# Kernel tuning notes

Hardware: AMD Instinct MI355X
Metric: run time of the kernel (lower is better)

The kernel has to match this reference:

```python
import jax, jax.numpy as jnp
import numpy as np

def setup_inputs() -> dict:
    key = jax.random.key(0)
    k1, k2, k3, k4 = jax.random.split(key, 4)
    B, T, D = 4, 4096, 256
    # xavier_normal_ with gain 0.002: std = 0.002 * sqrt(2/(D+D))
    std = 0.002 * np.sqrt(2.0 / (D + D))
    return {
        "x": jax.random.normal(k1, (B, T, D), dtype=jnp.float32),
        "W_k": jax.random.normal(k2, (D, D), dtype=jnp.float32) * std,
        "W_q": jax.random.normal(k3, (D, D), dtype=jnp.float32) * std,
        "W_v": jax.random.normal(k4, (D, D), dtype=jnp.float32) * std,
    }

def reference(x, W_k, W_q, W_v):
    # Projections: (B,T,D) @ (D,D) -> (B,T,D)
    K = jnp.einsum('btd,dk->btk', x, W_k)
    Q = jnp.einsum('btd,dq->btq', x, W_q)
    V = jnp.einsum('btd,dv->btv', x, W_v)
    # Note: original code has NO 1/sqrt(D) scaling.
    scores = jnp.einsum('bqd,bkd->bqk', Q, K)  # (B,T,T)
    attn = jax.nn.softmax(scores, axis=2)
    return jnp.einsum('bta,bav->btv', attn, V)
```

## Files before the change

### kernel.cpp

```cpp
#include <hip/hip_runtime.h>

typedef __attribute__((ext_vector_type(4))) float f32x4;
typedef __attribute__((ext_vector_type(8))) __bf16 bf16x8;
typedef __attribute__((ext_vector_type(4))) unsigned short u16x4;
typedef unsigned short u16;
typedef unsigned int u32;
typedef unsigned long long u64;

#define AS1 __attribute__((address_space(1)))
#define AS3 __attribute__((address_space(3)))

__device__ __forceinline__ void gload_lds16(const void* g, void* l) {
  __builtin_amdgcn_global_load_lds((const AS1 u32*)g, (AS3 u32*)l, 16, 0, 0);
}

__global__ __launch_bounds__(256) void k_flag(float* __restrict__ out, int n) {
  for (int i = blockIdx.x * 256 + threadIdx.x; i < n; i += gridDim.x * 256)
    out[i] = 1.0f;
}

__global__ __launch_bounds__(256) void k_cvt(const float* __restrict__ x,
                                             const float* __restrict__ Wk,
                                             const float* __restrict__ Wq,
                                             const float* __restrict__ Wv,
                                             __bf16* __restrict__ xb,
                                             __bf16* __restrict__ Wt) {
  int bx = blockIdx.x;
  if (bx < 2048) {
    int i = bx * 256 + threadIdx.x;
    const f32x4* p = (const f32x4*)x;
    f32x4 a = p[i * 2], b = p[i * 2 + 1];
    bf16x8 o;
    o[0] = (__bf16)a[0]; o[1] = (__bf16)a[1]; o[2] = (__bf16)a[2]; o[3] = (__bf16)a[3];
    o[4] = (__bf16)b[0]; o[5] = (__bf16)b[1]; o[6] = (__bf16)b[2]; o[7] = (__bf16)b[3];
    ((bf16x8*)xb)[i] = o;
  } else {
    int z = (bx - 2048) >> 8;
    const float* W = z == 0 ? Wk : (z == 1 ? Wq : Wv);
    int i = ((bx - 2048) & 255) * 256 + threadIdx.x;
    int n = i >> 8, k = i & 255;
    Wt[z * 65536 + i] = (__bf16)W[k * 256 + n];
  }
}

__global__ __launch_bounds__(256) void k_proj(const __bf16* __restrict__ xb,
                                              const __bf16* __restrict__ Wt,
                                              __bf16* __restrict__ Kb,
                                              __bf16* __restrict__ Qb,
                                              __bf16* __restrict__ Vt) {
  __shared__ __bf16 As[128 * 64];
  __shared__ __bf16 Bs[128 * 64];
  int tid = threadIdx.x;
  int lane = tid & 63, w = tid >> 6;
  int l15 = lane & 15, l4 = lane >> 4;
  int m0 = blockIdx.x * 128, n0 = blockIdx.y * 128;
  int z = blockIdx.z;
  const __bf16* Wz = Wt + z * 65536;
  int wm = (w & 1) * 64, wn = (w >> 1) * 64;
  f32x4 acc[4][4];
  for (int a = 0; a < 4; ++a)
    for (int b = 0; b < 4; ++b) acc[a][b] = (f32x4){0.f, 0.f, 0.f, 0.f};

  for (int k0 = 0; k0 < 256; k0 += 64) {
    __syncthreads();
    for (int it = 0; it < 4; ++it) {
      int id = it * 256 + tid;
      int r = id >> 3, c = id & 7, sc = c ^ (r & 7);
      gload_lds16(xb + (u64)(m0 + r) * 256 + k0 + sc * 8, (char*)As + id * 16);
    }
    for (int it = 0; it < 4; ++it) {
      int id = it * 256 + tid;
      int r = id >> 3, c = id & 7, sc = c ^ (r & 7);
      gload_lds16(Wz + (u64)(n0 + r) * 256 + k0 + sc * 8, (char*)Bs + id * 16);
    }
    asm volatile("s_waitcnt vmcnt(0)" ::: "memory");
    __syncthreads();
    for (int ks = 0; ks < 2; ++ks) {
      bf16x8 af[4], bg[4];
      for (int mf = 0; mf < 4; ++mf) {
        int m = wm + mf * 16 + l15;
        int ch = (ks * 4 + l4) ^ (m & 7);
        af[mf] = *(const bf16x8*)((const char*)As + m * 128 + ch * 16);
      }
      for (int nf = 0; nf < 4; ++nf) {
        int n = wn + nf * 16 + l15;
        int ch = (ks * 4 + l4) ^ (n & 7);
        bg[nf] = *(const bf16x8*)((const char*)Bs + n * 128 + ch * 16);
      }
      for (int mf = 0; mf < 4; ++mf)
        for (int nf = 0; nf < 4; ++nf)
          acc[mf][nf] = __builtin_amdgcn_mfma_f32_16x16x32_bf16(af[mf], bg[nf],
                                                                acc[mf][nf], 0, 0, 0);
    }
  }
  if (z != 2) {
    __bf16* C = z == 0 ? Kb : Qb;
    for (int mf = 0; mf < 4; ++mf)
      for (int nf = 0; nf < 4; ++nf)
        for (int r = 0; r < 4; ++r) {
          int m = m0 + wm + mf * 16 + l4 * 4 + r;
          int n = n0 + wn + nf * 16 + l15;
          C[(u64)m * 256 + n] = (__bf16)acc[mf][nf][r];
        }
  } else {
    int bb = m0 >> 12;
    for (int mf = 0; mf < 4; ++mf)
      for (int nf = 0; nf < 4; ++nf) {
        int n = n0 + wn + nf * 16 + l15;
        int tb = (m0 & 4095) + wm + mf * 16 + l4 * 4;
        u16x4 pk;
        for (int r = 0; r < 4; ++r) {
          __bf16 hh = (__bf16)acc[mf][nf][r];
          pk[r] = __builtin_bit_cast(u16, hh);
        }
        *(u16x4*)(Vt + (u64)bb * 1048576 + (u64)n * 4096 + tb) = pk;
      }
  }
}

#define KVB 32
__global__ __launch_bounds__(256) void k_attn(const __bf16* __restrict__ Qb,
                                              const __bf16* __restrict__ Kb,
                                              const __bf16* __restrict__ Vt,
                                              float* __restrict__ Out) {
  extern __shared__ char smem[];
  __bf16* Ks0 = (__bf16*)smem;
  __bf16* Ks1 = (__bf16*)(smem + 16384);
  __bf16* Vs0 = (__bf16*)(smem + 32768);
  __bf16* Vs1 = (__bf16*)(smem + 49152);
  __bf16* Ps  = (__bf16*)(smem + 65536);
  float*  Ls  = (float*)(smem + 69632);
  int tid = threadIdx.x, lane = tid & 63, w = tid >> 6;
  int l15 = lane & 15, l4 = lane >> 4;
  int s = w & 1, h = w >> 1;
  int id8 = blockIdx.x & 7, slot = blockIdx.x >> 3;
  int b = id8 >> 1;
  int q0 = (((id8 & 1) << 5) | slot) << 6;
  const __bf16* Kbb = Kb + (u64)b * 4096 * 256;
  const __bf16* Vtb = Vt + (u64)b * 1048576;

  bf16x8 qf[2][8];
  for (int mf = 0; mf < 2; ++mf) {
    const __bf16* Qrow = Qb + (u64)(b * 4096 + q0 + s * 32 + mf * 16 + l15) * 256;
    for (int ks = 0; ks < 8; ++ks) qf[mf][ks] = *(const bf16x8*)(Qrow + ks * 32 + l4 * 8);
  }

  f32x4 oacc[4][4];
  for (int a = 0; a < 4; ++a)
    for (int c = 0; c < 4; ++c) oacc[a][c] = (f32x4){0.f, 0.f, 0.f, 0.f};
  float lp[2][4] = {{0.f, 0.f, 0.f, 0.f}, {0.f, 0.f, 0.f, 0.f}};

  auto stageK = [&](int kv0, __bf16* dst) {
    for (int it = 0; it < 4; ++it) {
      int id = it * 256 + tid;
      int r = id >> 5, c = id & 31, sc = c ^ (r & 7);
      gload_lds16(Kbb + (u64)(kv0 + r) * 256 + sc * 8, (char*)dst + id * 16);
    }
  };
  auto stageV = [&](int kv0, __bf16* dst) {
    for (int it = 0; it < 4; ++it) {
      int id = it * 256 + tid;
      int d = id >> 2, c = id & 3, sc = c ^ (d & 3);
      gload_lds16(Vtb + (u64)d * 4096 + kv0 + sc * 8, (char*)dst + id * 16);
    }
  };

  stageK(0, Ks0);
  stageV(0, Vs0);
  asm volatile("s_waitcnt vmcnt(0)" ::: "memory");
  __syncthreads();

  for (int t = 0; t < 128; ++t) {
    __bf16* Kc = (t & 1) ? Ks1 : Ks0;
    __bf16* Vc = (t & 1) ? Vs1 : Vs0;
    __bf16* Kn = (t & 1) ? Ks0 : Ks1;
    __bf16* Vn = (t & 1) ? Vs0 : Vs1;
    if (t < 127) { stageK((t + 1) * KVB, Kn); stageV((t + 1) * KVB, Vn); }

    int kr = h * 16 + l15;
    f32x4 sa0 = (f32x4){0.f, 0.f, 0.f, 0.f}, sa1 = sa0, sb0 = sa0, sb1 = sa0;
    for (int ks = 0; ks < 8; ks += 2) {
      int ch0 = (ks * 4 + l4) ^ (kr & 7);
      int ch1 = ((ks + 1) * 4 + l4) ^ (kr & 7);
      bf16x8 kf0 = *(const bf16x8*)((const char*)Kc + kr * 512 + ch0 * 16);
      bf16x8 kf1 = *(const bf16x8*)((const char*)Kc + kr * 512 + ch1 * 16);
      sa0 = __builtin_amdgcn_mfma_f32_16x16x32_bf16(qf[0][ks], kf0, sa0, 0, 0, 0);
      sa1 = __builtin_amdgcn_mfma_f32_16x16x32_bf16(qf[1][ks], kf0, sa1, 0, 0, 0);
      sb0 = __builtin_amdgcn_mfma_f32_16x16x32_bf16(qf[0][ks + 1], kf1, sb0, 0, 0, 0);
      sb1 = __builtin_amdgcn_mfma_f32_16x16x32_bf16(qf[1][ks + 1], kf1, sb1, 0, 0, 0);
    }
    f32x4 sv[2] = {sa0 + sb0, sa1 + sb1};

    for (int mf = 0; mf < 2; ++mf)
      for (int r = 0; r < 4; ++r) {
        float p = __expf(sv[mf][r]);
        lp[mf][r] += p;
        int row = s * 32 + mf * 16 + l4 * 4 + r;
        int cs = (h * 2 + (l15 >> 3)) ^ l4;
        Ps[row * 32 + cs * 8 + (l15 & 7)] = (__bf16)p;
      }
    asm volatile("s_waitcnt lgkmcnt(0)\n\ts_barrier" ::: "memory");

    bf16x8 vf[4];
    for (int nf = 0; nf < 4; ++nf) {
      int d = w * 64 + nf * 16 + l15;
      int vc = l4 ^ (d & 3);
      vf[nf] = *(const bf16x8*)((const char*)Vc + d * 64 + vc * 16);
    }
    for (int mf = 0; mf < 4; ++mf) {
      int qr = mf * 16 + l15;
      int ch = l4 ^ ((l15 >> 2) & 3);
      bf16x8 pa = *(const bf16x8*)(Ps + qr * 32 + ch * 8);
      for (int nf = 0; nf < 4; ++nf)
        oacc[mf][nf] = __builtin_amdgcn_mfma_f32_16x16x32_bf16(pa, vf[nf], oacc[mf][nf], 0, 0, 0);
    }
    asm volatile("s_waitcnt vmcnt(0) lgkmcnt(0)\n\ts_barrier" ::: "memory");
  }

  for (int m = 1; m < 16; m <<= 1)
    for (int mf = 0; mf < 2; ++mf)
      for (int r = 0; r < 4; ++r) lp[mf][r] += __shfl_xor(lp[mf][r], m, 64);
  if (l15 == 0)
    for (int mf = 0; mf < 2; ++mf)
      for (int r = 0; r < 4; ++r)
        Ls[h * 64 + s * 32 + mf * 16 + l4 * 4 + r] = lp[mf][r];
  __syncthreads();

  float* Ob = Out + (u64)(b * 4096 + q0) * 256;
  for (int mf = 0; mf < 4; ++mf)
    for (int r = 0; r < 4; ++r) {
      int row = mf * 16 + l4 * 4 + r;
      float inv = 1.0f / (Ls[row] + Ls[64 + row]);
      for (int nf = 0; nf < 4; ++nf)
        Ob[(u64)row * 256 + w * 64 + nf * 16 + l15] = oacc[mf][nf][r] * inv;
    }
}

extern "C" void kernel_launch(void* const* d_in, const int* in_sizes, int n_in,
                              void* d_out, int out_size, void* d_ws, size_t ws_size,
                              hipStream_t stream) {
  const float* x  = (const float*)d_in[0];
  const float* Wk = (const float*)d_in[1];
  const float* Wq = (const float*)d_in[2];
  const float* Wv = (const float*)d_in[3];
  float* out = (float*)d_out;
  char* ws = (char*)d_ws;

  const size_t NEEDED = 25559040;
  if (ws_size < NEEDED) {
    k_flag<<<1024, 256, 0, stream>>>(out, out_size);
    return;
  }
  __bf16* Wt = (__bf16*)ws;
  __bf16* Kb = (__bf16*)(ws + 393216);
  __bf16* Qb = (__bf16*)(ws + 8781824);
  __bf16* Vt = (__bf16*)(ws + 17170432);
  __bf16* xb = (__bf16*)d_out;

  k_cvt<<<2816, 256, 0, stream>>>(x, Wk, Wq, Wv, xb, Wt);
  k_proj<<<dim3(128, 2, 3), 256, 0, stream>>>(xb, Wt, Kb, Qb, Vt);
  k_attn<<<256, 256, 70144, stream>>>(Qb, Kb, Vt, out);
}
```

Measured before the change: 214.4 us.

## Specialize attention warps into QK and PV groups, fuse x conversion into projection

The attention kernel now runs 8 waves: four compute QK^T and exp into a double-buffered P tile while the other four consume the previous step's P against V, so the two matmul phases overlap across waves with one barrier per step. The fp32-to-bf16 conversion of x moves into the projection GEMM's load path, removing a separate pass and the intermediate buffer. Projection tiles drop the XOR swizzle and async LDS loads in favour of padded shared memory and register-staged loads, and V is written transposed with swapped MFMA operands. The cost is more LDS, higher register pressure at 512 threads, and synchronous global loads in the projection.

```diff
diff --git a/kernel.cpp b/kernel.cpp
--- a/kernel.cpp
+++ b/kernel.cpp
@@ -2,7 +2,6 @@
 
 typedef __attribute__((ext_vector_type(4))) float f32x4;
 typedef __attribute__((ext_vector_type(8))) __bf16 bf16x8;
-typedef __attribute__((ext_vector_type(4))) unsigned short u16x4;
 typedef unsigned short u16;
 typedef unsigned int u32;
 typedef unsigned long long u64;
@@ -19,37 +18,23 @@
     out[i] = 1.0f;
 }
 
-__global__ __launch_bounds__(256) void k_cvt(const float* __restrict__ x,
-                                             const float* __restrict__ Wk,
-                                             const float* __restrict__ Wq,
-                                             const float* __restrict__ Wv,
-                                             __bf16* __restrict__ xb,
-                                             __bf16* __restrict__ Wt) {
-  int bx = blockIdx.x;
-  if (bx < 2048) {
-    int i = bx * 256 + threadIdx.x;
-    const f32x4* p = (const f32x4*)x;
-    f32x4 a = p[i * 2], b = p[i * 2 + 1];
-    bf16x8 o;
-    o[0] = (__bf16)a[0]; o[1] = (__bf16)a[1]; o[2] = (__bf16)a[2]; o[3] = (__bf16)a[3];
-    o[4] = (__bf16)b[0]; o[5] = (__bf16)b[1]; o[6] = (__bf16)b[2]; o[7] = (__bf16)b[3];
-    ((bf16x8*)xb)[i] = o;
-  } else {
-    int z = (bx - 2048) >> 8;
-    const float* W = z == 0 ? Wk : (z == 1 ? Wq : Wv);
-    int i = ((bx - 2048) & 255) * 256 + threadIdx.x;
-    int n = i >> 8, k = i & 255;
-    Wt[z * 65536 + i] = (__bf16)W[k * 256 + n];
-  }
-}
-
-__global__ __launch_bounds__(256) void k_proj(const __bf16* __restrict__ xb,
+__global__ __launch_bounds__(256) void k_cvt_w(const float* __restrict__ Wk,
+                                               const float* __restrict__ Wq,
+                                               const float* __restrict__ Wv,
+                                               __bf16* __restrict__ Wt) {
+  const float* W = blockIdx.y == 0 ? Wk : (blockIdx.y == 1 ? Wq : Wv);
+  int i = blockIdx.x * 256 + threadIdx.x;
+  int n = i >> 8, k = i & 255;
+  Wt[blockIdx.y * 65536 + i] = (__bf16)W[k * 256 + n];
+}
+
+__global__ __launch_bounds__(256) void k_proj(const float* __restrict__ x,
                                               const __bf16* __restrict__ Wt,
                                               __bf16* __restrict__ Kb,
                                               __bf16* __restrict__ Qb,
                                               __bf16* __restrict__ Vt) {
-  __shared__ __bf16 As[128 * 64];
-  __shared__ __bf16 Bs[128 * 64];
+  __shared__ __bf16 As[128][72];
+  __shared__ __bf16 Bs[128][72];
   int tid = threadIdx.x;
   int lane = tid & 63, w = tid >> 6;
   int l15 = lane & 15, l4 = lane >> 4;
@@ -64,33 +49,36 @@
   for (int k0 = 0; k0 < 256; k0 += 64) {
     __syncthreads();
     for (int it = 0; it < 4; ++it) {
-      int id = it * 256 + tid;
-      int r = id >> 3, c = id & 7, sc = c ^ (r & 7);
-      gload_lds16(xb + (u64)(m0 + r) * 256 + k0 + sc * 8, (char*)As + id * 16);
+      int id = it * 256 + tid, r = id >> 3, c = id & 7;
+      const float* src = x + (u64)(m0 + r) * 256 + k0 + c * 8;
+      f32x4 a = *(const f32x4*)src, b2 = *(const f32x4*)(src + 4);
+      bf16x8 o;
+      o[0] = (__bf16)a[0];  o[1] = (__bf16)a[1];  o[2] = (__bf16)a[2];  o[3] = (__bf16)a[3];
+      o[4] = (__bf16)b2[0]; o[5] = (__bf16)b2[1]; o[6] = (__bf16)b2[2]; o[7] = (__bf16)b2[3];
+      *(bf16x8*)&As[r][c * 8] = o;
     }
     for (int it = 0; it < 4; ++it) {
-      int id = it * 256 + tid;
-      int r = id >> 3, c = id & 7, sc = c ^ (r & 7);
-      gload_lds16(Wz + (u64)(n0 + r) * 256 + k0 + sc * 8, (char*)Bs + id * 16);
-    }
-    asm volatile("s_waitcnt vmcnt(0)" ::: "memory");
+      int id = it * 256 + tid, r = id >> 3, c = id & 7;
+      *(bf16x8*)&Bs[r][c * 8] = *(const bf16x8*)(Wz + (u64)(n0 + r) * 256 + k0 + c * 8);
+    }
     __syncthreads();
     for (int ks = 0; ks < 2; ++ks) {
       bf16x8 af[4], bg[4];
-      for (int mf = 0; mf < 4; ++mf) {
-        int m = wm + mf * 16 + l15;
-        int ch = (ks * 4 + l4) ^ (m & 7);
-        af[mf] = *(const bf16x8*)((const char*)As + m * 128 + ch * 16);
-      }
-      for (int nf = 0; nf < 4; ++nf) {
-        int n = wn + nf * 16 + l15;
-        int ch = (ks * 4 + l4) ^ (n & 7);
-        bg[nf] = *(const bf16x8*)((const char*)Bs + n * 128 + ch * 16);
-      }
       for (int mf = 0; mf < 4; ++mf)
-        for (int nf = 0; nf < 4; ++nf)
-          acc[mf][nf] = __builtin_amdgcn_mfma_f32_16x16x32_bf16(af[mf], bg[nf],
-                                                                acc[mf][nf], 0, 0, 0);
+        af[mf] = *(const bf16x8*)&As[wm + mf * 16 + l15][(ks * 4 + l4) * 8];
+      for (int nf = 0; nf < 4; ++nf)
+        bg[nf] = *(const bf16x8*)&Bs[wn + nf * 16 + l15][(ks * 4 + l4) * 8];
+      if (z != 2) {
+        for (int mf = 0; mf < 4; ++mf)
+          for (int nf = 0; nf < 4; ++nf)
+            acc[mf][nf] = __builtin_amdgcn_mfma_f32_16x16x32_bf16(af[mf], bg[nf],
+                                                                  acc[mf][nf], 0, 0, 0);
+      } else {
+        for (int mf = 0; mf < 4; ++mf)
+          for (int nf = 0; nf < 4; ++nf)
+            acc[mf][nf] = __builtin_amdgcn_mfma_f32_16x16x32_bf16(bg[nf], af[mf],
+                                                                  acc[mf][nf], 0, 0, 0);
+      }
     }
   }
   if (z != 2) {
@@ -105,34 +93,26 @@
   } else {
     int bb = m0 >> 12;
     for (int mf = 0; mf < 4; ++mf)
-      for (int nf = 0; nf < 4; ++nf) {
-        int n = n0 + wn + nf * 16 + l15;
-        int tb = (m0 & 4095) + wm + mf * 16 + l4 * 4;
-        u16x4 pk;
+      for (int nf = 0; nf < 4; ++nf)
         for (int r = 0; r < 4; ++r) {
-          __bf16 hh = (__bf16)acc[mf][nf][r];
-          pk[r] = __builtin_bit_cast(u16, hh);
-        }
-        *(u16x4*)(Vt + (u64)bb * 1048576 + (u64)n * 4096 + tb) = pk;
-      }
+          int n = n0 + wn + nf * 16 + l4 * 4 + r;
+          int t = (m0 & 4095) + wm + mf * 16 + l15;
+          Vt[(u64)bb * 1048576 + (u64)n * 4096 + t] = (__bf16)acc[mf][nf][r];
+        }
   }
 }
 
 #define KVB 32
-__global__ __launch_bounds__(256) void k_attn(const __bf16* __restrict__ Qb,
-                                              const __bf16* __restrict__ Kb,
-                                              const __bf16* __restrict__ Vt,
-                                              float* __restrict__ Out) {
+__global__ __launch_bounds__(512, 2) void k_attn(const __bf16* __restrict__ Qb,
+                                                 const __bf16* __restrict__ Kb,
+                                                 const __bf16* __restrict__ Vt,
+                                                 float* __restrict__ Out) {
   extern __shared__ char smem[];
-  __bf16* Ks0 = (__bf16*)smem;
-  __bf16* Ks1 = (__bf16*)(smem + 16384);
-  __bf16* Vs0 = (__bf16*)(smem + 32768);
-  __bf16* Vs1 = (__bf16*)(smem + 49152);
-  __bf16* Ps  = (__bf16*)(smem + 65536);
-  float*  Ls  = (float*)(smem + 69632);
+  float* Ls = (float*)(smem + 73728);
   int tid = threadIdx.x, lane = tid & 63, w = tid >> 6;
   int l15 = lane & 15, l4 = lane >> 4;
-  int s = w & 1, h = w >> 1;
+  bool isQK = (w < 4);
+  int s = w & 1, h = (w >> 1) & 1, w4 = w - 4;
   int id8 = blockIdx.x & 7, slot = blockIdx.x >> 3;
   int b = id8 >> 1;
   int q0 = (((id8 & 1) << 5) | slot) << 6;
@@ -140,100 +120,110 @@
   const __bf16* Vtb = Vt + (u64)b * 1048576;
 
   bf16x8 qf[2][8];
-  for (int mf = 0; mf < 2; ++mf) {
-    const __bf16* Qrow = Qb + (u64)(b * 4096 + q0 + s * 32 + mf * 16 + l15) * 256;
-    for (int ks = 0; ks < 8; ++ks) qf[mf][ks] = *(const bf16x8*)(Qrow + ks * 32 + l4 * 8);
-  }
+  if (isQK)
+    for (int mf = 0; mf < 2; ++mf) {
+      const __bf16* Qrow = Qb + (u64)(b * 4096 + q0 + s * 32 + mf * 16 + l15) * 256;
+      for (int ks = 0; ks < 8; ++ks) qf[mf][ks] = *(const bf16x8*)(Qrow + ks * 32 + l4 * 8);
+    }
 
   f32x4 oacc[4][4];
   for (int a = 0; a < 4; ++a)
     for (int c = 0; c < 4; ++c) oacc[a][c] = (f32x4){0.f, 0.f, 0.f, 0.f};
   float lp[2][4] = {{0.f, 0.f, 0.f, 0.f}, {0.f, 0.f, 0.f, 0.f}};
 
-  auto stageK = [&](int kv0, __bf16* dst) {
-    for (int it = 0; it < 4; ++it) {
-      int id = it * 256 + tid;
+  auto stageK = [&](int kv0, char* dst) {
+    for (int it = 0; it < 2; ++it) {
+      int id = it * 512 + tid;
       int r = id >> 5, c = id & 31, sc = c ^ (r & 7);
-      gload_lds16(Kbb + (u64)(kv0 + r) * 256 + sc * 8, (char*)dst + id * 16);
+      gload_lds16(Kbb + (u64)(kv0 + r) * 256 + sc * 8, dst + id * 16);
     }
   };
-  auto stageV = [&](int kv0, __bf16* dst) {
-    for (int it = 0; it < 4; ++it) {
-      int id = it * 256 + tid;
+  auto stageV = [&](int kv0, char* dst) {
+    for (int it = 0; it < 2; ++it) {
+      int id = it * 512 + tid;
       int d = id >> 2, c = id & 3, sc = c ^ (d & 3);
-      gload_lds16(Vtb + (u64)d * 4096 + kv0 + sc * 8, (char*)dst + id * 16);
+      gload_lds16(Vtb + (u64)d * 4096 + kv0 + sc * 8, dst + id * 16);
     }
   };
 
-  stageK(0, Ks0);
-  stageV(0, Vs0);
+  stageK(0, smem);
   asm volatile("s_waitcnt vmcnt(0)" ::: "memory");
   __syncthreads();
 
-  for (int t = 0; t < 128; ++t) {
-    __bf16* Kc = (t & 1) ? Ks1 : Ks0;
-    __bf16* Vc = (t & 1) ? Vs1 : Vs0;
-    __bf16* Kn = (t & 1) ? Ks0 : Ks1;
-    __bf16* Vn = (t & 1) ? Vs0 : Vs1;
-    if (t < 127) { stageK((t + 1) * KVB, Kn); stageV((t + 1) * KVB, Vn); }
-
-    int kr = h * 16 + l15;
-    f32x4 sa0 = (f32x4){0.f, 0.f, 0.f, 0.f}, sa1 = sa0, sb0 = sa0, sb1 = sa0;
-    for (int ks = 0; ks < 8; ks += 2) {
-      int ch0 = (ks * 4 + l4) ^ (kr & 7);
-      int ch1 = ((ks + 1) * 4 + l4) ^ (kr & 7);
-      bf16x8 kf0 = *(const bf16x8*)((const char*)Kc + kr * 512 + ch0 * 16);
-      bf16x8 kf1 = *(const bf16x8*)((const char*)Kc + kr * 512 + ch1 * 16);
-      sa0 = __builtin_amdgcn_mfma_f32_16x16x32_bf16(qf[0][ks], kf0, sa0, 0, 0, 0);
-      sa1 = __builtin_amdgcn_mfma_f32_16x16x32_bf16(qf[1][ks], kf0, sa1, 0, 0, 0);
-      sb0 = __builtin_amdgcn_mfma_f32_16x16x32_bf16(qf[0][ks + 1], kf1, sb0, 0, 0, 0);
-      sb1 = __builtin_amdgcn_mfma_f32_16x16x32_bf16(qf[1][ks + 1], kf1, sb1, 0, 0, 0);
-    }
-    f32x4 sv[2] = {sa0 + sb0, sa1 + sb1};
-
-    for (int mf = 0; mf < 2; ++mf)
+  for (int t = 0; t <= 128; ++t) {
+    char* KsC = smem + (t & 1) * 16384;
+    char* VsP = smem + 32768 + ((t + 1) & 1) * 16384;
+    char* PsC = smem + 65536 + (t & 1) * 4096;
+    char* PsP = smem + 65536 + ((t + 1) & 1) * 4096;
+    if (t < 127) stageK((t + 1) * KVB, smem + ((t + 1) & 1) * 16384);
+    if (t < 128) stageV(t * KVB, smem + 32768 + (t & 1) * 16384);
+
+    if (isQK) {
+      if (t < 128) {
+        int kr = h * 16 + l15;
+        f32x4 sa0 = (f32x4){0.f, 0.f, 0.f, 0.f}, sa1 = sa0, sb0 = sa0, sb1 = sa0;
+        for (int ks = 0; ks < 8; ks += 2) {
+          int ch0 = (ks * 4 + l4) ^ (kr & 7);
+          int ch1 = ((ks + 1) * 4 + l4) ^ (kr & 7);
+          bf16x8 kf0 = *(const bf16x8*)(KsC + kr * 512 + ch0 * 16);
+          bf16x8 kf1 = *(const bf16x8*)(KsC + kr * 512 + ch1 * 16);
+          sa0 = __builtin_amdgcn_mfma_f32_16x16x32_bf16(qf[0][ks], kf0, sa0, 0, 0, 0);
+          sa1 = __builtin_amdgcn_mfma_f32_16x16x32_bf16(qf[1][ks], kf0, sa1, 0, 0, 0);
+          sb0 = __builtin_amdgcn_mfma_f32_16x16x32_bf16(qf[0][ks + 1], kf1, sb0, 0, 0, 0);
+          sb1 = __builtin_amdgcn_mfma_f32_16x16x32_bf16(qf[1][ks + 1], kf1, sb1, 0, 0, 0);
+        }
+        f32x4 sv[2] = {sa0 + sb0, sa1 + sb1};
+        for (int mf = 0; mf < 2; ++mf)
+          for (int r = 0; r < 4; ++r) {
+            float p = __expf(sv[mf][r]);
+            lp[mf][r] += p;
+            int row = s * 32 + mf * 16 + l4 * 4 + r;
+            int cs = (h * 2 + (l15 >> 3)) ^ l4;
+            *(__bf16*)(PsC + row * 64 + cs * 16 + (l15 & 7) * 2) = (__bf16)p;
+          }
+      }
+    } else {
+      if (t >= 1) {
+        bf16x8 vf[4];
+        for (int nf = 0; nf < 4; ++nf) {
+          int d = w4 * 64 + nf * 16 + l15;
+          int vc = l4 ^ (d & 3);
+          vf[nf] = *(const bf16x8*)(VsP + d * 64 + vc * 16);
+        }
+        for (int mf = 0; mf < 4; ++mf) {
+          int qr = mf * 16 + l15;
+          int ch = l4 ^ ((l15 >> 2) & 3);
+          bf16x8 pa = *(const bf16x8*)(PsP + qr * 64 + ch * 16);
+          for (int nf = 0; nf < 4; ++nf)
+            oacc[mf][nf] = __builtin_amdgcn_mfma_f32_16x16x32_bf16(pa, vf[nf],
+                                                                   oacc[mf][nf], 0, 0, 0);
+        }
+      }
+    }
+    if (t < 128)
+      asm volatile("s_waitcnt vmcnt(0) lgkmcnt(0)\n\ts_barrier" ::: "memory");
+  }
+
+  if (isQK) {
+    for (int m = 1; m < 16; m <<= 1)
+      for (int mf = 0; mf < 2; ++mf)
+        for (int r = 0; r < 4; ++r) lp[mf][r] += __shfl_xor(lp[mf][r], m, 64);
+    if (l15 == 0)
+      for (int mf = 0; mf < 2; ++mf)
+        for (int r = 0; r < 4; ++r)
+          Ls[h * 64 + s * 32 + mf * 16 + l4 * 4 + r] = lp[mf][r];
+  }
+  __syncthreads();
+  if (!isQK) {
+    float* Ob = Out + (u64)(b * 4096 + q0) * 256;
+    for (int mf = 0; mf < 4; ++mf)
       for (int r = 0; r < 4; ++r) {
-        float p = __expf(sv[mf][r]);
-        lp[mf][r] += p;
-        int row = s * 32 + mf * 16 + l4 * 4 + r;
-        int cs = (h * 2 + (l15 >> 3)) ^ l4;
-        Ps[row * 32 + cs * 8 + (l15 & 7)] = (__bf16)p;
-      }
-    asm volatile("s_waitcnt lgkmcnt(0)\n\ts_barrier" ::: "memory");
-
-    bf16x8 vf[4];
-    for (int nf = 0; nf < 4; ++nf) {
-      int d = w * 64 + nf * 16 + l15;
-      int vc = l4 ^ (d & 3);
-      vf[nf] = *(const bf16x8*)((const char*)Vc + d * 64 + vc * 16);
-    }
-    for (int mf = 0; mf < 4; ++mf) {
-      int qr = mf * 16 + l15;
-      int ch = l4 ^ ((l15 >> 2) & 3);
-      bf16x8 pa = *(const bf16x8*)(Ps + qr * 32 + ch * 8);
-      for (int nf = 0; nf < 4; ++nf)
-        oacc[mf][nf] = __builtin_amdgcn_mfma_f32_16x16x32_bf16(pa, vf[nf], oacc[mf][nf], 0, 0, 0);
-    }
-    asm volatile("s_waitcnt vmcnt(0) lgkmcnt(0)\n\ts_barrier" ::: "memory");
-  }
-
-  for (int m = 1; m < 16; m <<= 1)
-    for (int mf = 0; mf < 2; ++mf)
-      for (int r = 0; r < 4; ++r) lp[mf][r] += __shfl_xor(lp[mf][r], m, 64);
-  if (l15 == 0)
-    for (int mf = 0; mf < 2; ++mf)
-      for (int r = 0; r < 4; ++r)
-        Ls[h * 64 + s * 32 + mf * 16 + l4 * 4 + r] = lp[mf][r];
-  __syncthreads();
-
-  float* Ob = Out + (u64)(b * 4096 + q0) * 256;
-  for (int mf = 0; mf < 4; ++mf)
-    for (int r = 0; r < 4; ++r) {
-      int row = mf * 16 + l4 * 4 + r;
-      float inv = 1.0f / (Ls[row] + Ls[64 + row]);
-      for (int nf = 0; nf < 4; ++nf)
-        Ob[(u64)row * 256 + w * 64 + nf * 16 + l15] = oacc[mf][nf][r] * inv;
-    }
+        int row = mf * 16 + l4 * 4 + r;
+        float inv = 1.0f / (Ls[row] + Ls[64 + row]);
+        for (int nf = 0; nf < 4; ++nf)
+          Ob[(u64)row * 256 + w4 * 64 + nf * 16 + l15] = oacc[mf][nf][r] * inv;
+      }
+  }
 }
 
 extern "C" void kernel_launch(void* const* d_in, const int* in_sizes, int n_in,
@@ -255,9 +245,8 @@
   __bf16* Kb = (__bf16*)(ws + 393216);
   __bf16* Qb = (__bf16*)(ws + 8781824);
   __bf16* Vt = (__bf16*)(ws + 17170432);
-  __bf16* xb = (__bf16*)d_out;
-
-  k_cvt<<<2816, 256, 0, stream>>>(x, Wk, Wq, Wv, xb, Wt);
-  k_proj<<<dim3(128, 2, 3), 256, 0, stream>>>(xb, Wt, Kb, Qb, Vt);
-  k_attn<<<256, 256, 70144, stream>>>(Qb, Kb, Vt, out);
-}
+
+  k_cvt_w<<<dim3(256, 3), 256, 0, stream>>>(Wk, Wq, Wv, Wt);
+  k_proj<<<dim3(128, 2, 3), 256, 0, stream>>>(x, Wt, Kb, Qb, Vt);
+  k_attn<<<256, 512, 74240, stream>>>(Qb, Kb, Vt, out);
+}
```

New measurement: 188.7 us. -12.0%, faster.
